# Optimization experiments

Measured on AMD Instinct MI355X. Metric: run time of the kernel, lower is better.

## Reference

```python
import jax, jax.numpy as jnp
import numpy as np

HIDDEN = 1024
HEADS = 16
HEAD_DIM = HIDDEN // HEADS
SCALE = 1.0 / (HEAD_DIM ** 0.5)


def setup_inputs() -> dict:
    key = jax.random.key(0)
    k1, k2, k3 = jax.random.split(key, 3)
    B, S = 2, 2048
    x = jax.random.normal(k1, (B, S, HIDDEN), dtype=jnp.float32)
    # torch Linear weights: (out_features, in_features), y = x @ W.T
    qkv_w = jax.random.normal(k2, (3 * HIDDEN, HIDDEN), dtype=jnp.float32) * (HIDDEN ** -0.5)
    out_w = jax.random.normal(k3, (HIDDEN, HIDDEN), dtype=jnp.float32) * (HIDDEN ** -0.5)
    return {"x": x, "qkv_w": qkv_w, "out_w": out_w}


def reference(x, qkv_w, out_w):
    B, S, H = x.shape
    qkv = jnp.einsum('bsh,oh->bso', x, qkv_w)  # [B,S,3H]
    q, k, v = jnp.split(qkv, 3, axis=-1)
    def heads(t):
        return t.reshape(B, S, HEADS, HEAD_DIM).transpose(0, 2, 1, 3)  # [B,nh,S,hd]
    q, k, v = heads(q), heads(k), heads(v)
    scores = jnp.einsum('bhqd,bhkd->bhqk', q, k) * SCALE  # [B,nh,S,S]
    attn = jax.nn.softmax(scores, axis=-1)
    out = jnp.einsum('bhqk,bhkd->bhqd', attn, v)  # [B,nh,S,hd]
    out = out.transpose(0, 2, 1, 3).reshape(B, S, H)
    return jnp.einsum('bsh,oh->bso', out, out_w)
```

## Files before the change

### kernel.cpp

```cpp
#include <hip/hip_runtime.h>
#include <hip/hip_bf16.h>

#define BB 2
#define SS 2048
#define HH 1024
#define NH 16
#define HD 64
#define MM (BB * SS)
#define N_QKV (3 * HH)
#define KK HH

typedef __attribute__((ext_vector_type(8))) short short8;
typedef __attribute__((ext_vector_type(4))) float floatx4;
typedef __attribute__((ext_vector_type(16))) float floatx16;

#define MFMA16(a, b, c) __builtin_amdgcn_mfma_f32_16x16x32_bf16(a, b, c, 0, 0, 0)
#define MFMA32(a, b, c) __builtin_amdgcn_mfma_f32_32x32x16_bf16(a, b, c, 0, 0, 0)

__device__ __forceinline__ unsigned short f2bf(float f) {
  unsigned int u = __builtin_bit_cast(unsigned int, f);
  u += 0x7FFFu + ((u >> 16) & 1u);
  return (unsigned short)(u >> 16);
}

__device__ __forceinline__ float fexp2(float x) {
#if __has_builtin(__builtin_amdgcn_exp2f)
  return __builtin_amdgcn_exp2f(x);
#else
  float r; asm("v_exp_f32 %0, %1" : "=v"(r) : "v"(x)); return r;
#endif
}

__device__ __forceinline__ unsigned int pack2(float lo, float hi) {
  unsigned int a = __builtin_bit_cast(unsigned int, lo);
  unsigned int b = __builtin_bit_cast(unsigned int, hi);
  a += 0x7FFFu + ((a >> 16) & 1u);
  b += 0x7FFFu + ((b >> 16) & 1u);
  return __builtin_amdgcn_perm(b, a, 0x07060302u);
}

__device__ __forceinline__ unsigned int pack2e(float lo, float hi) {
  unsigned int a = __builtin_bit_cast(unsigned int, lo) + 0x8000u;
  unsigned int b = __builtin_bit_cast(unsigned int, hi) + 0x8000u;
  return __builtin_amdgcn_perm(b, a, 0x07060302u);
}

__device__ __forceinline__ uint4 cvt8(float4 lo, float4 hi) {
  uint4 u;
  u.x = pack2(lo.x, lo.y);
  u.y = pack2(lo.z, lo.w);
  u.z = pack2(hi.x, hi.y);
  u.w = pack2(hi.z, hi.w);
  return u;
}

__global__ __launch_bounds__(256) void gemm_qkv(const float* __restrict__ X,
                                                const float* __restrict__ Wf,
                                                unsigned short* __restrict__ qb,
                                                unsigned short* __restrict__ kb,
                                                unsigned short* __restrict__ vtb) {
  __shared__ __attribute__((aligned(16))) unsigned short As[128 * 32];
  __shared__ __attribute__((aligned(16))) unsigned short Bs[128 * 32];
  const int tid = threadIdx.x;
  const int wave = tid >> 6, lane = tid & 63;
  const int quad = lane >> 4, lc = lane & 15;
  const int m0 = blockIdx.y * 128, n0 = blockIdx.x * 128;
  const int wm = (wave >> 1) * 64, wn = (wave & 1) * 64;

  floatx4 acc[4][4];
#pragma unroll
  for (int i = 0; i < 4; i++)
#pragma unroll
    for (int j = 0; j < 4; j++) acc[i][j] = (floatx4){0.f, 0.f, 0.f, 0.f};

  const float* Ag = X + (size_t)(m0 + (tid >> 2)) * KK + (tid & 3) * 8;
  const float* Bg = Wf + (size_t)(n0 + (tid >> 2)) * KK + (tid & 3) * 8;
  unsigned short* AsW = As + wave * 512 + lane * 8;
  unsigned short* BsW = Bs + wave * 512 + lane * 8;

  float4 a0l = *(const float4*)(Ag),                     a0h = *(const float4*)(Ag + 4);
  float4 a1l = *(const float4*)(Ag + (size_t)64 * KK),   a1h = *(const float4*)(Ag + (size_t)64 * KK + 4);
  float4 b0l = *(const float4*)(Bg),                     b0h = *(const float4*)(Bg + 4);
  float4 b1l = *(const float4*)(Bg + (size_t)64 * KK),   b1h = *(const float4*)(Bg + (size_t)64 * KK + 4);

  for (int it = 0; it < KK / 32; ++it) {
    __syncthreads();
    *(uint4*)(AsW) = cvt8(a0l, a0h);
    *(uint4*)(AsW + 2048) = cvt8(a1l, a1h);
    *(uint4*)(BsW) = cvt8(b0l, b0h);
    *(uint4*)(BsW + 2048) = cvt8(b1l, b1h);
    if (it + 1 < KK / 32) {
      int k0 = (it + 1) * 32;
      a0l = *(const float4*)(Ag + k0);                    a0h = *(const float4*)(Ag + k0 + 4);
      a1l = *(const float4*)(Ag + k0 + (size_t)64 * KK);  a1h = *(const float4*)(Ag + k0 + (size_t)64 * KK + 4);
      b0l = *(const float4*)(Bg + k0);                    b0h = *(const float4*)(Bg + k0 + 4);
      b1l = *(const float4*)(Bg + k0 + (size_t)64 * KK);  b1h = *(const float4*)(Bg + k0 + (size_t)64 * KK + 4);
    }
    __syncthreads();
    short8 af[4], bf[4];
#pragma unroll
    for (int i = 0; i < 4; i++) {
      af[i] = *(const short8*)(As + (wm + i * 16 + lc) * 32 + quad * 8);
      bf[i] = *(const short8*)(Bs + (wn + i * 16 + lc) * 32 + quad * 8);
    }
#pragma unroll
    for (int i = 0; i < 4; i++)
#pragma unroll
      for (int j = 0; j < 4; j++) acc[i][j] = MFMA16(af[i], bf[j], acc[i][j]);
  }

  const float QSCALE = 0.125f * 1.44269504f;
#pragma unroll
  for (int j = 0; j < 4; j++) {
    int n = n0 + wn + j * 16 + lc;
#pragma unroll
    for (int i = 0; i < 4; i++) {
      int mbase = m0 + wm + i * 16 + quad * 4;
      int b = mbase >> 11;
      int s0 = mbase & 2047;
      if (n < HH) {
        int h = n >> 6, d = n & 63;
#pragma unroll
        for (int r = 0; r < 4; r++)
          qb[(((size_t)(b * NH + h) * SS + s0 + r) * HD) + d] = f2bf(acc[i][j][r] * QSCALE);
      } else if (n < 2 * HH) {
        int n2 = n - HH; int h = n2 >> 6, d = n2 & 63;
#pragma unroll
        for (int r = 0; r < 4; r++)
          kb[(((size_t)(b * NH + h) * SS + s0 + r) * HD) + d] = f2bf(acc[i][j][r]);
      } else {
        int n2 = n - 2 * HH; int h = n2 >> 6, d = n2 & 63;
        ushort4 p;
        p.x = f2bf(acc[i][j][0]); p.y = f2bf(acc[i][j][1]);
        p.z = f2bf(acc[i][j][2]); p.w = f2bf(acc[i][j][3]);
        *(ushort4*)(vtb + ((size_t)(b * NH + h) * HD + d) * SS + s0) = p;
      }
    }
  }
}

__device__ __forceinline__ int co(int row, int c16) {
  return row * 64 + ((c16 ^ ((row ^ (row >> 3)) & 7)) << 3);
}

__global__ __launch_bounds__(256, 2) void attn_kernel(const unsigned short* __restrict__ qg,
                                                      const unsigned short* __restrict__ kg,
                                                      const unsigned short* __restrict__ vtg,
                                                      unsigned short* __restrict__ og) {
  __shared__ __attribute__((aligned(16))) unsigned short Sall[16384];
  unsigned short* Qs = Sall;
  unsigned short* Ks = Sall + 8192;
  unsigned short* Vs = Sall + 12288;

  const int tid = threadIdx.x;
  const int w = tid >> 6, lane = tid & 63;
  const int hl = lane >> 5, c = lane & 31;
  const int q0 = blockIdx.x * 128;
  const int head = blockIdx.y, b = blockIdx.z;

  const unsigned short* qbase = qg + (size_t)(b * NH + head) * SS * HD;
  const unsigned short* kbase = kg + (size_t)(b * NH + head) * SS * HD;
  const unsigned short* vbase = vtg + (size_t)(b * NH + head) * HD * SS;

  {
    int row = tid >> 3, cc = tid & 7;
#pragma unroll
    for (int s = 0; s < 4; s++)
      *(uint4*)(Qs + co(row + 32 * s, cc)) =
          *(const uint4*)(qbase + (size_t)(q0 + row + 32 * s) * HD + cc * 8);
  }

  const int frow = tid >> 3, fc = tid & 7;
  uint4 k0r = *(const uint4*)(kbase + (size_t)frow * HD + fc * 8);
  uint4 k1r = *(const uint4*)(kbase + (size_t)(frow + 32) * HD + fc * 8);
  uint4 v0r = *(const uint4*)(vbase + (size_t)frow * SS + fc * 8);
  uint4 v1r = *(const uint4*)(vbase + (size_t)(frow + 32) * SS + fc * 8);

  floatx16 oacc0, oacc1, lacc;
#pragma unroll
  for (int i = 0; i < 16; i++) { oacc0[i] = 0.f; oacc1[i] = 0.f; lacc[i] = 0.f; }

  short8 ones;
#pragma unroll
  for (int i = 0; i < 8; i++) ones[i] = (short)0x3F80;

  short8 qa[4];

  for (int kt = 0; kt < SS; kt += 64) {
    __syncthreads();
    *(uint4*)(Ks + co(frow, fc)) = k0r;
    *(uint4*)(Ks + co(frow + 32, fc)) = k1r;
    *(uint4*)(Vs + co(frow, fc)) = v0r;
    *(uint4*)(Vs + co(frow + 32, fc)) = v1r;
    if (kt + 64 < SS) {
      k0r = *(const uint4*)(kbase + (size_t)(kt + 64 + frow) * HD + fc * 8);
      k1r = *(const uint4*)(kbase + (size_t)(kt + 96 + frow) * HD + fc * 8);
      v0r = *(const uint4*)(vbase + (size_t)frow * SS + kt + 64 + fc * 8);
      v1r = *(const uint4*)(vbase + (size_t)(frow + 32) * SS + kt + 64 + fc * 8);
    }
    __syncthreads();

    if (kt == 0) {
#pragma unroll
      for (int ks = 0; ks < 4; ks++)
        qa[ks] = *(const short8*)(Qs + co(w * 32 + c, ks * 2 + hl));
    }

    floatx16 sacc0, sacc1;
#pragma unroll
    for (int i = 0; i < 16; i++) { sacc0[i] = 0.f; sacc1[i] = 0.f; }
#pragma unroll
    for (int ks = 0; ks < 4; ks++) {
      short8 ka0 = *(const short8*)(Ks + co(c, ks * 2 + hl));
      short8 ka1 = *(const short8*)(Ks + co(32 + c, ks * 2 + hl));
      sacc0 = MFMA32(ka0, qa[ks], sacc0);
      sacc1 = MFMA32(ka1, qa[ks], sacc1);
    }

    short8 pb[4];
#pragma unroll
    for (int kb = 0; kb < 4; kb++) {
      const floatx16& s = (kb < 2) ? sacc0 : sacc1;
      int base = (kb & 1) * 8;
      unsigned int u0 = pack2e(fexp2(s[base + 0]), fexp2(s[base + 1]));
      unsigned int u1 = pack2e(fexp2(s[base + 2]), fexp2(s[base + 3]));
      unsigned int u2 = pack2e(fexp2(s[base + 4]), fexp2(s[base + 5]));
      unsigned int u3 = pack2e(fexp2(s[base + 6]), fexp2(s[base + 7]));
      uint4 u = {u0, u1, u2, u3};
      pb[kb] = __builtin_bit_cast(short8, u);
    }

#pragma unroll
    for (int kb = 0; kb < 4; kb++) {
      uint2 lo0 = *(const uint2*)(Vs + co(c, 2 * kb) + 4 * hl);
      uint2 hi0 = *(const uint2*)(Vs + co(c, 2 * kb + 1) + 4 * hl);
      uint4 a0 = {lo0.x, lo0.y, hi0.x, hi0.y};
      short8 va0 = __builtin_bit_cast(short8, a0);
      uint2 lo1 = *(const uint2*)(Vs + co(32 + c, 2 * kb) + 4 * hl);
      uint2 hi1 = *(const uint2*)(Vs + co(32 + c, 2 * kb + 1) + 4 * hl);
      uint4 a1 = {lo1.x, lo1.y, hi1.x, hi1.y};
      short8 va1 = __builtin_bit_cast(short8, a1);
      oacc0 = MFMA32(va0, pb[kb], oacc0);
      oacc1 = MFMA32(va1, pb[kb], oacc1);
      lacc = MFMA32(ones, pb[kb], lacc);
    }
  }

  __syncthreads();
  unsigned short* sc = Sall + w * 2176;
  float inv = 1.0f / lacc[0];
#pragma unroll
  for (int t = 0; t < 8; t++) {
    int d0 = ((2 * t) & 3) + 8 * (t >> 1) + 4 * hl;
    *(unsigned int*)(sc + c * 68 + d0) = pack2e(oacc0[2 * t] * inv, oacc0[2 * t + 1] * inv);
    *(unsigned int*)(sc + c * 68 + 32 + d0) = pack2e(oacc1[2 * t] * inv, oacc1[2 * t + 1] * inv);
  }
  {
    int ql = lane >> 1, hf = lane & 1;
    size_t row = (size_t)(b * SS + q0 + w * 32 + ql);
    unsigned short* dst = og + row * HH + head * 64 + hf * 32;
    const unsigned short* srcp = sc + ql * 68 + hf * 32;
#pragma unroll
    for (int s = 0; s < 4; s++) {
      uint2 a = *(const uint2*)(srcp + s * 8);
      uint2 bq = *(const uint2*)(srcp + s * 8 + 4);
      uint4 v = {a.x, a.y, bq.x, bq.y};
      *(uint4*)(dst + s * 8) = v;
    }
  }
}

__global__ __launch_bounds__(256) void gemm_out(const unsigned short* __restrict__ A,
                                                const float* __restrict__ Wf,
                                                float* __restrict__ C) {
  __shared__ __attribute__((aligned(16))) unsigned short As[128 * 32];
  __shared__ __attribute__((aligned(16))) unsigned short Bs[64 * 32];
  const int tid = threadIdx.x;
  const int wave = tid >> 6, lane = tid & 63;
  const int quad = lane >> 4, lc = lane & 15;
  const int m0 = blockIdx.y * 128, n0 = blockIdx.x * 64;
  const int wm = (wave >> 1) * 64, wn = (wave & 1) * 32;

  floatx4 acc[4][2];
#pragma unroll
  for (int i = 0; i < 4; i++)
#pragma unroll
    for (int j = 0; j < 2; j++) acc[i][j] = (floatx4){0.f, 0.f, 0.f, 0.f};

  const unsigned short* Ag = A + (size_t)(m0 + (tid >> 2)) * KK + (tid & 3) * 8;
  const float* Bg = Wf + (size_t)(n0 + (tid >> 2)) * KK + (tid & 3) * 8;
  unsigned short* AsW = As + wave * 512 + lane * 8;
  unsigned short* BsW = Bs + wave * 512 + lane * 8;

  uint4 a0 = *(const uint4*)(Ag);
  uint4 a1 = *(const uint4*)(Ag + (size_t)64 * KK);
  float4 b0l = *(const float4*)(Bg), b0h = *(const float4*)(Bg + 4);

  for (int it = 0; it < KK / 32; ++it) {
    __syncthreads();
    *(uint4*)(AsW) = a0;
    *(uint4*)(AsW + 2048) = a1;
    *(uint4*)(BsW) = cvt8(b0l, b0h);
    if (it + 1 < KK / 32) {
      int k0 = (it + 1) * 32;
      a0 = *(const uint4*)(Ag + k0);
      a1 = *(const uint4*)(Ag + k0 + (size_t)64 * KK);
      b0l = *(const float4*)(Bg + k0);
      b0h = *(const float4*)(Bg + k0 + 4);
    }
    __syncthreads();
    short8 af[4], bf[2];
#pragma unroll
    for (int i = 0; i < 4; i++)
      af[i] = *(const short8*)(As + (wm + i * 16 + lc) * 32 + quad * 8);
#pragma unroll
    for (int j = 0; j < 2; j++)
      bf[j] = *(const short8*)(Bs + (wn + j * 16 + lc) * 32 + quad * 8);
#pragma unroll
    for (int i = 0; i < 4; i++)
#pragma unroll
      for (int j = 0; j < 2; j++) acc[i][j] = MFMA16(af[i], bf[j], acc[i][j]);
  }

#pragma unroll
  for (int i = 0; i < 4; i++)
#pragma unroll
    for (int j = 0; j < 2; j++) {
      int m = m0 + wm + i * 16 + quad * 4;
      int n = n0 + wn + j * 16 + lc;
#pragma unroll
      for (int r = 0; r < 4; r++) C[(size_t)(m + r) * HH + n] = acc[i][j][r];
    }
}

extern "C" void kernel_launch(void* const* d_in, const int* in_sizes, int n_in,
                              void* d_out, int out_size, void* d_ws, size_t ws_size,
                              hipStream_t stream) {
  const float* x = (const float*)d_in[0];
  const float* qkv_w = (const float*)d_in[1];
  const float* out_w = (const float*)d_in[2];
  float* out = (float*)d_out;

  char* ws = (char*)d_ws;
  unsigned short* qb  = (unsigned short*)(ws + 0);
  unsigned short* kb  = (unsigned short*)(ws + 8388608);
  unsigned short* vtb = (unsigned short*)(ws + 16777216);
  unsigned short* ao  = (unsigned short*)(ws + 25165824);

  gemm_qkv<<<dim3(N_QKV / 128, MM / 128), dim3(256), 0, stream>>>(x, qkv_w, qb, kb, vtb);
  attn_kernel<<<dim3(SS / 128, NH, BB), dim3(256), 0, stream>>>(qb, kb, vtb, ao);
  gemm_out<<<dim3(HH / 64, MM / 128), dim3(256), 0, stream>>>(ao, out_w, out);
}
```

Measured before the change: 193.7 us.

## Pre-cast inputs and weights to bf16 and load GEMM tiles directly into LDS

Adds a separate cast kernel that converts x, qkv_w (when the workspace is large enough) and out_w to bf16 in workspace buffers. The GEMM kernels then stage their tiles with global_load_lds direct-to-LDS loads instead of loading fp32, converting in registers and writing to LDS. Conversion now uses the v_cvt_pk_bf16_f32 instruction. The goal is to halve GEMM operand traffic and cut VALU and register work. The cost is extra kernel launches, a full read and write pass for the casts, and the loss of register prefetch double-buffering.

```diff
diff --git a/kernel.cpp b/kernel.cpp
--- a/kernel.cpp
+++ b/kernel.cpp
@@ -31,31 +31,45 @@
 #endif
 }
 
-__device__ __forceinline__ unsigned int pack2(float lo, float hi) {
-  unsigned int a = __builtin_bit_cast(unsigned int, lo);
-  unsigned int b = __builtin_bit_cast(unsigned int, hi);
-  a += 0x7FFFu + ((a >> 16) & 1u);
-  b += 0x7FFFu + ((b >> 16) & 1u);
-  return __builtin_amdgcn_perm(b, a, 0x07060302u);
-}
-
 __device__ __forceinline__ unsigned int pack2e(float lo, float hi) {
   unsigned int a = __builtin_bit_cast(unsigned int, lo) + 0x8000u;
   unsigned int b = __builtin_bit_cast(unsigned int, hi) + 0x8000u;
   return __builtin_amdgcn_perm(b, a, 0x07060302u);
 }
 
-__device__ __forceinline__ uint4 cvt8(float4 lo, float4 hi) {
+__device__ __forceinline__ unsigned int cvtpk(float lo, float hi) {
+  unsigned int r;
+  asm("v_cvt_pk_bf16_f32 %0, %1, %2" : "=v"(r) : "v"(lo), "v"(hi));
+  return r;
+}
+
+__device__ __forceinline__ uint4 cvt8pk(float4 lo, float4 hi) {
   uint4 u;
-  u.x = pack2(lo.x, lo.y);
-  u.y = pack2(lo.z, lo.w);
-  u.z = pack2(hi.x, hi.y);
-  u.w = pack2(hi.z, hi.w);
+  u.x = cvtpk(lo.x, lo.y);
+  u.y = cvtpk(lo.z, lo.w);
+  u.z = cvtpk(hi.x, hi.y);
+  u.w = cvtpk(hi.z, hi.w);
   return u;
 }
 
-__global__ __launch_bounds__(256) void gemm_qkv(const float* __restrict__ X,
+__device__ __forceinline__ void gload_lds16(const void* g, void* l) {
+  __builtin_amdgcn_global_load_lds((const __attribute__((address_space(1))) void*)g,
+                                   (__attribute__((address_space(3))) void*)l,
+                                   16, 0, 0);
+}
+
+__global__ __launch_bounds__(256) void cast_g(const float* __restrict__ s,
+                                              unsigned short* __restrict__ d) {
+  size_t i = (size_t)blockIdx.x * 256 + threadIdx.x;
+  float4 lo = *(const float4*)(s + i * 8);
+  float4 hi = *(const float4*)(s + i * 8 + 4);
+  *(uint4*)(d + i * 8) = cvt8pk(lo, hi);
+}
+
+template <int BPRE>
+__global__ __launch_bounds__(256) void gemm_qkv(const unsigned short* __restrict__ Xb,
                                                 const float* __restrict__ Wf,
+                                                const unsigned short* __restrict__ Wb,
                                                 unsigned short* __restrict__ qb,
                                                 unsigned short* __restrict__ kb,
                                                 unsigned short* __restrict__ vtb) {
@@ -66,6 +80,7 @@
   const int quad = lane >> 4, lc = lane & 15;
   const int m0 = blockIdx.y * 128, n0 = blockIdx.x * 128;
   const int wm = (wave >> 1) * 64, wn = (wave & 1) * 64;
+  const int sr = tid >> 2, sc = (tid & 3) * 8;
 
   floatx4 acc[4][4];
 #pragma unroll
@@ -73,28 +88,37 @@
 #pragma unroll
     for (int j = 0; j < 4; j++) acc[i][j] = (floatx4){0.f, 0.f, 0.f, 0.f};
 
-  const float* Ag = X + (size_t)(m0 + (tid >> 2)) * KK + (tid & 3) * 8;
-  const float* Bg = Wf + (size_t)(n0 + (tid >> 2)) * KK + (tid & 3) * 8;
-  unsigned short* AsW = As + wave * 512 + lane * 8;
+  const unsigned short* Axp = Xb + (size_t)(m0 + sr) * KK + sc;
+  unsigned short* AsD = As + wave * 512;
+  unsigned short* BsD = Bs + wave * 512;
+
+  const unsigned short* Bxp = nullptr;
+  const float* Bg = nullptr;
+  float4 b0l, b0h, b1l, b1h;
   unsigned short* BsW = Bs + wave * 512 + lane * 8;
-
-  float4 a0l = *(const float4*)(Ag),                     a0h = *(const float4*)(Ag + 4);
-  float4 a1l = *(const float4*)(Ag + (size_t)64 * KK),   a1h = *(const float4*)(Ag + (size_t)64 * KK + 4);
-  float4 b0l = *(const float4*)(Bg),                     b0h = *(const float4*)(Bg + 4);
-  float4 b1l = *(const float4*)(Bg + (size_t)64 * KK),   b1h = *(const float4*)(Bg + (size_t)64 * KK + 4);
+  if constexpr (BPRE) {
+    Bxp = Wb + (size_t)(n0 + sr) * KK + sc;
+  } else {
+    Bg = Wf + (size_t)(n0 + sr) * KK + sc;
+    b0l = *(const float4*)(Bg);                    b0h = *(const float4*)(Bg + 4);
+    b1l = *(const float4*)(Bg + (size_t)64 * KK);  b1h = *(const float4*)(Bg + (size_t)64 * KK + 4);
+  }
 
   for (int it = 0; it < KK / 32; ++it) {
-    __syncthreads();
-    *(uint4*)(AsW) = cvt8(a0l, a0h);
-    *(uint4*)(AsW + 2048) = cvt8(a1l, a1h);
-    *(uint4*)(BsW) = cvt8(b0l, b0h);
-    *(uint4*)(BsW + 2048) = cvt8(b1l, b1h);
-    if (it + 1 < KK / 32) {
-      int k0 = (it + 1) * 32;
-      a0l = *(const float4*)(Ag + k0);                    a0h = *(const float4*)(Ag + k0 + 4);
-      a1l = *(const float4*)(Ag + k0 + (size_t)64 * KK);  a1h = *(const float4*)(Ag + k0 + (size_t)64 * KK + 4);
-      b0l = *(const float4*)(Bg + k0);                    b0h = *(const float4*)(Bg + k0 + 4);
-      b1l = *(const float4*)(Bg + k0 + (size_t)64 * KK);  b1h = *(const float4*)(Bg + k0 + (size_t)64 * KK + 4);
+    const int k0 = it * 32;
+    __syncthreads();
+    gload_lds16(Axp + k0, AsD);
+    gload_lds16(Axp + (size_t)64 * KK + k0, AsD + 2048);
+    if constexpr (BPRE) {
+      gload_lds16(Bxp + k0, BsD);
+      gload_lds16(Bxp + (size_t)64 * KK + k0, BsD + 2048);
+    } else {
+      *(uint4*)(BsW) = cvt8pk(b0l, b0h);
+      *(uint4*)(BsW + 2048) = cvt8pk(b1l, b1h);
+      if (it + 1 < KK / 32) {
+        b0l = *(const float4*)(Bg + k0 + 32);                    b0h = *(const float4*)(Bg + k0 + 36);
+        b1l = *(const float4*)(Bg + k0 + 32 + (size_t)64 * KK);  b1h = *(const float4*)(Bg + k0 + 36 + (size_t)64 * KK);
+      }
     }
     __syncthreads();
     short8 af[4], bf[4];
@@ -271,7 +295,7 @@
 }
 
 __global__ __launch_bounds__(256) void gemm_out(const unsigned short* __restrict__ A,
-                                                const float* __restrict__ Wf,
+                                                const unsigned short* __restrict__ Wb,
                                                 float* __restrict__ C) {
   __shared__ __attribute__((aligned(16))) unsigned short As[128 * 32];
   __shared__ __attribute__((aligned(16))) unsigned short Bs[64 * 32];
@@ -280,6 +304,7 @@
   const int quad = lane >> 4, lc = lane & 15;
   const int m0 = blockIdx.y * 128, n0 = blockIdx.x * 64;
   const int wm = (wave >> 1) * 64, wn = (wave & 1) * 32;
+  const int sr = tid >> 2, sc = (tid & 3) * 8;
 
   floatx4 acc[4][2];
 #pragma unroll
@@ -287,27 +312,17 @@
 #pragma unroll
     for (int j = 0; j < 2; j++) acc[i][j] = (floatx4){0.f, 0.f, 0.f, 0.f};
 
-  const unsigned short* Ag = A + (size_t)(m0 + (tid >> 2)) * KK + (tid & 3) * 8;
-  const float* Bg = Wf + (size_t)(n0 + (tid >> 2)) * KK + (tid & 3) * 8;
-  unsigned short* AsW = As + wave * 512 + lane * 8;
-  unsigned short* BsW = Bs + wave * 512 + lane * 8;
-
-  uint4 a0 = *(const uint4*)(Ag);
-  uint4 a1 = *(const uint4*)(Ag + (size_t)64 * KK);
-  float4 b0l = *(const float4*)(Bg), b0h = *(const float4*)(Bg + 4);
+  const unsigned short* Axp = A + (size_t)(m0 + sr) * KK + sc;
+  const unsigned short* Bxp = Wb + (size_t)(n0 + sr) * KK + sc;
+  unsigned short* AsD = As + wave * 512;
+  unsigned short* BsD = Bs + wave * 512;
 
   for (int it = 0; it < KK / 32; ++it) {
-    __syncthreads();
-    *(uint4*)(AsW) = a0;
-    *(uint4*)(AsW + 2048) = a1;
-    *(uint4*)(BsW) = cvt8(b0l, b0h);
-    if (it + 1 < KK / 32) {
-      int k0 = (it + 1) * 32;
-      a0 = *(const uint4*)(Ag + k0);
-      a1 = *(const uint4*)(Ag + k0 + (size_t)64 * KK);
-      b0l = *(const float4*)(Bg + k0);
-      b0h = *(const float4*)(Bg + k0 + 4);
-    }
+    const int k0 = it * 32;
+    __syncthreads();
+    gload_lds16(Axp + k0, AsD);
+    gload_lds16(Axp + (size_t)64 * KK + k0, AsD + 2048);
+    gload_lds16(Bxp + k0, BsD);
     __syncthreads();
     short8 af[4], bf[2];
 #pragma unroll
@@ -345,9 +360,21 @@
   unsigned short* qb  = (unsigned short*)(ws + 0);
   unsigned short* kb  = (unsigned short*)(ws + 8388608);
   unsigned short* vtb = (unsigned short*)(ws + 16777216);
-  unsigned short* ao  = (unsigned short*)(ws + 25165824);
-
-  gemm_qkv<<<dim3(N_QKV / 128, MM / 128), dim3(256), 0, stream>>>(x, qkv_w, qb, kb, vtb);
+  unsigned short* xb  = (unsigned short*)(ws + 25165824);
+  unsigned short* ao  = xb;
+  unsigned short* wob = qb;
+
+  const bool big = ws_size >= 40ull * 1024 * 1024;
+  unsigned short* w1b = big ? (unsigned short*)(ws + 33554432) : nullptr;
+
+  cast_g<<<dim3(MM * KK / 2048), dim3(256), 0, stream>>>(x, xb);
+  if (big) {
+    cast_g<<<dim3(N_QKV * KK / 2048), dim3(256), 0, stream>>>(qkv_w, w1b);
+    gemm_qkv<1><<<dim3(N_QKV / 128, MM / 128), dim3(256), 0, stream>>>(xb, qkv_w, w1b, qb, kb, vtb);
+  } else {
+    gemm_qkv<0><<<dim3(N_QKV / 128, MM / 128), dim3(256), 0, stream>>>(xb, qkv_w, nullptr, qb, kb, vtb);
+  }
   attn_kernel<<<dim3(SS / 128, NH, BB), dim3(256), 0, stream>>>(qb, kb, vtb, ao);
-  gemm_out<<<dim3(HH / 64, MM / 128), dim3(256), 0, stream>>>(ao, out_w, out);
-}
+  cast_g<<<dim3(HH * KK / 2048), dim3(256), 0, stream>>>(out_w, wob);
+  gemm_out<<<dim3(HH / 64, MM / 128), dim3(256), 0, stream>>>(ao, wob, out);
+}
```

Result: slower. 199.7 us (+3.1%).
